# Kernel tuning notes

Hardware: AMD Instinct MI355X
Metric: run time of the kernel (lower is better)

Reference implementation:

```python
import jax, jax.numpy as jnp
from jax import lax
import numpy as np

EPS = 4e-3            # geoopt float32 ball boundary eps
MAXNORM = 1.0 - EPS   # c = 1 Poincare ball


def _norm(x):
    return jnp.sqrt(jnp.maximum(jnp.sum(x * x, axis=-1, keepdims=True), 1e-15))


def expmap0(u):
    n = _norm(u)
    return jnp.tanh(n) * u / n


def projx(x):
    n = _norm(x)
    return jnp.where(n > MAXNORM, x * (MAXNORM / n), x)


def mobius_add(x, y):
    x2 = jnp.sum(x * x, -1, keepdims=True)
    y2 = jnp.sum(y * y, -1, keepdims=True)
    xy = jnp.sum(x * y, -1, keepdims=True)
    num = (1.0 + 2.0 * xy + y2) * x + (1.0 - x2) * y
    den = 1.0 + 2.0 * xy + x2 * y2
    return num / jnp.maximum(den, 1e-15)


def mamba_layer(x, inW, convW, convb, xpW, dtW, dtb, A_log, Dp, outW):
    # x: [B,T,H]; inW: [2*Din,H]; convW: [Din,K]; xpW: [R+2N,Din]; dtW: [Din,R]
    B, T, H = x.shape
    Din, N = A_log.shape
    K = convW.shape[-1]
    R = dtW.shape[-1]
    xz = jnp.einsum('bth,dh->btd', x, inW)              # [B,T,2*Din]
    xr, z = jnp.split(xz, 2, axis=-1)
    xc = lax.conv_general_dilated(jnp.transpose(xr, (0, 2, 1)), convW[:, None, :],
                                  (1,), [(K - 1, 0)], feature_group_count=Din)
    u = jax.nn.silu(jnp.transpose(xc + convb[None, :, None], (0, 2, 1)))  # [B,T,Din]
    x_dbl = jnp.einsum('btd,ed->bte', u, xpW)           # [B,T,R+2N]
    dt_r, Bm, Cm = x_dbl[..., :R], x_dbl[..., R:R + N], x_dbl[..., R + N:]
    dt = jax.nn.softplus(jnp.einsum('btr,dr->btd', dt_r, dtW) + dtb)      # [B,T,Din]
    A = -jnp.exp(A_log)                                 # [Din,N]
    dA = jnp.exp(dt[..., None] * A)                     # [B,T,Din,N]
    dBu = dt[..., None] * Bm[:, :, None, :] * u[..., None]

    def step(h, ins):
        dA_t, dBu_t, C_t = ins
        h = dA_t * h + dBu_t                            # [B,Din,N]
        return h, jnp.einsum('bdn,bn->bd', h, C_t)

    h0 = jnp.zeros((B, Din, N), x.dtype)
    _, ys = lax.scan(step, h0, (jnp.moveaxis(dA, 1, 0), jnp.moveaxis(dBu, 1, 0), jnp.moveaxis(Cm, 1, 0)))
    y = jnp.moveaxis(ys, 0, 1) + Dp * u                 # [B,T,Din]
    return jnp.einsum('btd,hd->bth', y * jax.nn.silu(z), outW)


def _encode(xs, inp_W, inp_b, in_proj_W, conv_W, conv_b, xproj_W, dt_W, dt_b, A_log, D_skip, out_W, outp_W, outp_b):
    # xs: [4,B,T,1]; params carry leading branch dim 4, then layer dim 3
    def branch(x, iW, ib, ipW, cW, cb, xpW, dW, db, Al, Dp, oW, opW, opb):
        h = jnp.einsum('bti,hi->bth', x, iW) + ib
        for l in range(ipW.shape[0]):
            h = mamba_layer(h, ipW[l], cW[l], cb[l], xpW[l], dW[l], db[l], Al[l], Dp[l], oW[l])
        return jnp.tanh(jnp.einsum('bth,eh->bte', h, opW) + opb)
    return jax.vmap(branch)(xs, inp_W, inp_b, in_proj_W, conv_W, conv_b, xproj_W, dt_W, dt_b, A_log, D_skip, out_W, outp_W, outp_b)


def setup_inputs() -> dict:
    key = jax.random.key(0)
    ks = jax.random.split(key, 24)
    Br, B, T, H, Din, N, K, R, E, L = 4, 32, 1024, 64, 128, 16, 4, 4, 32, 3

    def rn(k, shape, s=0.05):
        return jax.random.normal(k, shape, jnp.float32) * s

    A_init = jnp.log(jnp.arange(1, N + 1, dtype=jnp.float32))
    return {
        'trend': jax.random.normal(ks[0], (B, T, 1), jnp.float32),
        'seasonal_weekly': jax.random.normal(ks[1], (B, T, 1), jnp.float32),
        'seasonal_daily': jax.random.normal(ks[2], (B, T, 1), jnp.float32),
        'residual': jax.random.normal(ks[3], (B, T, 1), jnp.float32),
        'inp_W': rn(ks[4], (Br, H, 1), 0.5),
        'inp_b': rn(ks[5], (Br, H)),
        'in_proj_W': rn(ks[6], (Br, L, 2 * Din, H)),
        'conv_W': rn(ks[7], (Br, L, Din, K), 0.2),
        'conv_b': rn(ks[8], (Br, L, Din)),
        'xproj_W': rn(ks[9], (Br, L, R + 2 * N, Din)),
        'dt_W': rn(ks[10], (Br, L, Din, R), 0.2),
        'dt_b': rn(ks[11], (Br, L, Din), 0.5) - 4.0,  # softplus(dt_b) small
        'A_log': jnp.tile(A_init, (Br, L, Din, 1)) + rn(ks[12], (Br, L, Din, N), 0.01),
        'D_skip': jnp.ones((Br, L, Din), jnp.float32) + rn(ks[13], (Br, L, Din), 0.01),
        'out_W': rn(ks[14], (Br, L, H, Din)),
        'outp_W': rn(ks[15], (Br, E, H)),
        'outp_b': rn(ks[16], (Br, E)),
    }


def reference(trend, seasonal_weekly, seasonal_daily, residual, inp_W, inp_b, in_proj_W, conv_W, conv_b, xproj_W, dt_W, dt_b, A_log, D_skip, out_W, outp_W, outp_b):
    xs = jnp.stack([trend, seasonal_weekly, seasonal_daily, residual], 0)  # [4,B,T,1]
    z = _encode(xs, inp_W, inp_b, in_proj_W, conv_W, conv_b, xproj_W, dt_W, dt_b, A_log, D_skip, out_W, outp_W, outp_b)  # [4,B,T,E]
    zh = projx(expmap0(z))
    t, w, d, r = zh[0], zh[1], zh[2], zh[3]
    comb = projx(mobius_add(mobius_add(t, mobius_add(w, d)), r))
    # stacked [trend_h, weekly_h, daily_h, residual_h, combined_h]
    return jnp.stack([t, w, d, r, comb], 0)
```

## Files before the change

### kernel.cpp

```cpp
#include <hip/hip_runtime.h>
#include <math.h>

#define TT 1024
#define DIN 128
#define HH 64
#define NN 16
#define EE 32
#define LL 3
#define BB 32

__device__ __forceinline__ float siluf(float x) { return x / (1.f + __expf(-x)); }

typedef __attribute__((ext_vector_type(8))) short bf16x8;
typedef __attribute__((ext_vector_type(4))) float f32x4;

__device__ __forceinline__ void split2(float x, ushort& hi, ushort& lo) {
  unsigned u = __float_as_uint(x);
  hi = (ushort)(u >> 16);
  float rem = x - __uint_as_float((u >> 16) << 16);
  lo = (ushort)(__float_as_uint(rem) >> 16);
}

#define WXZ_N 196608
#define WXD_N 73728
#define WOUT_N 98304

__global__ __launch_bounds__(256) void k_presplit(
    const float* __restrict__ iprojW, const float* __restrict__ xprojW,
    const float* __restrict__ outW,
    ushort* __restrict__ WxzH, ushort* __restrict__ WxzL,
    ushort* __restrict__ WxdH, ushort* __restrict__ WxdL,
    ushort* __restrict__ WoH, ushort* __restrict__ WoL) {
  int idx = blockIdx.x * 256 + threadIdx.x;
  if (idx < WXZ_N) {
    ushort h, l;
    split2(iprojW[idx], h, l);
    WxzH[idx] = h; WxzL[idx] = l;
  }
  if (idx < WXD_N) {
    int k = idx & 127, r = (idx >> 7) % 48, bl = idx / (48 * 128);
    float v = (r < 36) ? xprojW[((size_t)(bl * 36 + r)) * 128 + k] : 0.f;
    ushort h, l;
    split2(v, h, l);
    WxdH[idx] = h; WxdL[idx] = l;
  }
  if (idx < WOUT_N) {
    ushort h, l;
    split2(outW[idx], h, l);
    WoH[idx] = h; WoL[idx] = l;
  }
}

__global__ __launch_bounds__(256) void k_xz(
    const float* __restrict__ x0, const float* __restrict__ x1,
    const float* __restrict__ x2, const float* __restrict__ x3,
    const float* __restrict__ h, const ushort* __restrict__ WH,
    const ushort* __restrict__ WL,
    const float* __restrict__ inpW, const float* __restrict__ inpb,
    float* __restrict__ xr, float* __restrict__ zb, int br0, int l) {
  __shared__ __align__(16) ushort Hh[64][72], Hl[64][72];
  const int tid = threadIdx.x;
  const int b  = blockIdx.y;
  const int t0 = blockIdx.x * 64;
  const int br = br0 + (b >> 5);
  const float* Hg = h + ((size_t)b * TT + t0) * HH;
  {
    const int row = tid >> 2, c0 = (tid & 3) * 16;
    float xv = 0.f;
    if (l == 0) {
      int bb = b & 31;
      const float* xp = (br == 0) ? x0 : (br == 1) ? x1 : (br == 2) ? x2 : x3;
      xv = xp[bb * TT + t0 + row];
    }
    #pragma unroll
    for (int q = 0; q < 4; ++q) {
      float4 hv;
      if (l == 0) {
        float4 w4 = *(const float4*)(inpW + br * HH + c0 + q * 4);
        float4 b4 = *(const float4*)(inpb + br * HH + c0 + q * 4);
        hv.x = xv * w4.x + b4.x; hv.y = xv * w4.y + b4.y;
        hv.z = xv * w4.z + b4.z; hv.w = xv * w4.w + b4.w;
      } else {
        hv = *(const float4*)(Hg + (size_t)row * HH + c0 + q * 4);
      }
      ushort h0,h1,h2,h3,l0,l1,l2,l3;
      split2(hv.x,h0,l0); split2(hv.y,h1,l1); split2(hv.z,h2,l2); split2(hv.w,h3,l3);
      *(ushort4*)&Hh[row][c0 + q*4] = make_ushort4(h0,h1,h2,h3);
      *(ushort4*)&Hl[row][c0 + q*4] = make_ushort4(l0,l1,l2,l3);
    }
  }
  __syncthreads();
  const int wave = tid >> 6, lane = tid & 63;
  const int quad = lane >> 4, l16 = lane & 15;
  const int nsub = (wave & 1) * 32, tsub = (wave >> 1) * 32;
  const size_t wbase = (size_t)(br * LL + l) * 256;
  for (int n0 = 0; n0 < 2 * DIN; n0 += 64) {
    f32x4 acc[2][2] = {};
    #pragma unroll
    for (int k0 = 0; k0 < 64; k0 += 32) {
      bf16x8 Ah[2], Al[2], Bh[2], Bl[2];
      #pragma unroll
      for (int i = 0; i < 2; ++i) {
        size_t ro = (wbase + n0 + nsub + i * 16 + l16) * 64 + k0 + quad * 8;
        Ah[i] = *(const bf16x8*)(WH + ro);
        Al[i] = *(const bf16x8*)(WL + ro);
        Bh[i] = *(const bf16x8*)&Hh[tsub + i*16 + l16][k0 + quad*8];
        Bl[i] = *(const bf16x8*)&Hl[tsub + i*16 + l16][k0 + quad*8];
      }
      #pragma unroll
      for (int i = 0; i < 2; ++i)
        #pragma unroll
        for (int j = 0; j < 2; ++j) {
          acc[i][j] = __builtin_amdgcn_mfma_f32_16x16x32_bf16(Ah[i], Bh[j], acc[i][j], 0, 0, 0);
          acc[i][j] = __builtin_amdgcn_mfma_f32_16x16x32_bf16(Ah[i], Bl[j], acc[i][j], 0, 0, 0);
          acc[i][j] = __builtin_amdgcn_mfma_f32_16x16x32_bf16(Al[i], Bh[j], acc[i][j], 0, 0, 0);
        }
    }
    #pragma unroll
    for (int i = 0; i < 2; ++i) {
      #pragma unroll
      for (int r = 0; r < 4; ++r) {
        int n = n0 + nsub + i*16 + quad*4 + r;
        float* dst = (n < DIN) ? (xr + ((size_t)b * DIN + n) * TT)
                               : (zb + ((size_t)b * DIN + (n - DIN)) * TT);
        #pragma unroll
        for (int j = 0; j < 2; ++j)
          dst[t0 + tsub + j*16 + l16] = acc[i][j][r];
      }
    }
  }
}

__global__ __launch_bounds__(256) void k_xdbl(
    const float* __restrict__ xr, const float* __restrict__ convW,
    const float* __restrict__ convb, const ushort* __restrict__ WH,
    const ushort* __restrict__ WL, const float* __restrict__ dtW,
    const float* __restrict__ dtb,
    float* __restrict__ u, float* __restrict__ dt,
    float* __restrict__ Bm, float* __restrict__ Cm,
    int br0, int l) {
  __shared__ __align__(16) float Xr[16][72];
  __shared__ __align__(16) float As2[32][65];
  __shared__ __align__(16) float Xs[40][68];
  const int tid = threadIdx.x;
  const int b  = blockIdx.y;
  const int t0 = blockIdx.x * 64;
  const int br = br0 + (b >> 5);
  const int rowk = tid >> 4, c4 = tid & 15;
  const int wave = tid >> 6, lane = tid & 63;
  const int quad = lane >> 4, l16 = lane & 15;
  const int tw = wave * 16;
  const size_t wb48 = (size_t)(br * LL + l) * 48 * 128;
  f32x4 acc[3] = {};
  for (int k0 = 0; k0 < DIN; k0 += 32) {
    #pragma unroll
    for (int ks = 0; ks < 32; ks += 16) {
      __syncthreads();
      {
        const float* src = xr + ((size_t)b * DIN + k0 + ks + rowk) * TT + t0;
        *(float4*)&Xr[rowk][4 + c4 * 4] = *(const float4*)(src + c4 * 4);
        if (tid < 16) {
          float4 hv = make_float4(0.f, 0.f, 0.f, 0.f);
          if (t0 > 0) hv = *(const float4*)(xr + ((size_t)b * DIN + k0 + ks + tid) * TT + t0 - 4);
          *(float4*)&Xr[tid][0] = hv;
        }
      }
      __syncthreads();
      {
        int d = k0 + ks + rowk;
        const float* w = convW + (size_t)((br * LL + l) * DIN + d) * 4;
        float w0 = w[0], w1 = w[1], w2 = w[2], w3 = w[3];
        float cb = convb[(br * LL + l) * DIN + d];
        int ic = c4 * 4;
        float4 Av = *(const float4*)&Xr[rowk][ic];
        float4 Bv = *(const float4*)&Xr[rowk][ic + 4];
        float o0 = siluf(Av.y*w0 + Av.z*w1 + Av.w*w2 + Bv.x*w3 + cb);
        float o1 = siluf(Av.z*w0 + Av.w*w1 + Bv.x*w2 + Bv.y*w3 + cb);
        float o2 = siluf(Av.w*w0 + Bv.x*w1 + Bv.y*w2 + Bv.z*w3 + cb);
        float o3 = siluf(Bv.x*w0 + Bv.y*w1 + Bv.z*w2 + Bv.w*w3 + cb);
        *(float4*)(u + ((size_t)b * DIN + d) * TT + t0 + ic) = make_float4(o0, o1, o2, o3);
        As2[ks + rowk][ic]     = o0;
        As2[ks + rowk][ic + 1] = o1;
        As2[ks + rowk][ic + 2] = o2;
        As2[ks + rowk][ic + 3] = o3;
      }
    }
    __syncthreads();
    ushort bh[8], bl[8];
    #pragma unroll
    for (int j = 0; j < 8; ++j) {
      split2(As2[quad * 8 + j][tw + l16], bh[j], bl[j]);
    }
    bf16x8 Bh = *(bf16x8*)bh, Bl = *(bf16x8*)bl;
    #pragma unroll
    for (int nf = 0; nf < 3; ++nf) {
      size_t ro = wb48 + (size_t)(nf * 16 + l16) * 128 + k0 + quad * 8;
      bf16x8 Whf = *(const bf16x8*)(WH + ro);
      bf16x8 Wlf = *(const bf16x8*)(WL + ro);
      acc[nf] = __builtin_amdgcn_mfma_f32_16x16x32_bf16(Whf, Bh, acc[nf], 0, 0, 0);
      acc[nf] = __builtin_amdgcn_mfma_f32_16x16x32_bf16(Whf, Bl, acc[nf], 0, 0, 0);
      acc[nf] = __builtin_amdgcn_mfma_f32_16x16x32_bf16(Wlf, Bh, acc[nf], 0, 0, 0);
    }
  }
  __syncthreads();
  #pragma unroll
  for (int nf = 0; nf < 3; ++nf) {
    #pragma unroll
    for (int r = 0; r < 4; ++r) {
      int n = nf * 16 + quad * 4 + r;
      if (n < 40) Xs[n][tw + l16] = acc[nf][r];
    }
  }
  __syncthreads();
  {
    int n = tid >> 4, i0 = (tid & 15) * 4;
    *(float4*)(Bm + ((size_t)b * NN + n) * TT + t0 + i0) = *(float4*)&Xs[4 + n][i0];
    *(float4*)(Cm + ((size_t)b * NN + n) * TT + t0 + i0) = *(float4*)&Xs[20 + n][i0];
  }
  {
    int d = tid >> 1, half = tid & 1;
    const float* wd = dtW + (size_t)((br * LL + l) * DIN + d) * 4;
    float w0 = wd[0], w1 = wd[1], w2 = wd[2], w3 = wd[3];
    float bias = dtb[(br * LL + l) * DIN + d];
    float* dtp = dt + ((size_t)b * DIN + d) * TT + t0 + half * 32;
    #pragma unroll
    for (int g8 = 0; g8 < 8; ++g8) {
      float o[4];
      #pragma unroll
      for (int q = 0; q < 4; ++q) {
        int i = half * 32 + g8 * 4 + q;
        float s = Xs[0][i]*w0 + Xs[1][i]*w1 + Xs[2][i]*w2 + Xs[3][i]*w3 + bias;
        float e = __expf(-fabsf(s));
        o[q] = fmaxf(s, 0.f) + __logf(1.f + e);
      }
      *(float4*)(dtp + g8*4) = make_float4(o[0], o[1], o[2], o[3]);
    }
  }
}

__global__ __launch_bounds__(256) void k_scan1(
    float* __restrict__ dtc, const float* __restrict__ u,
    const float* __restrict__ Bm, const float* __restrict__ Cm,
    const float* __restrict__ A_log, const float* __restrict__ D_skip,
    float* __restrict__ Hloc, float* __restrict__ g, float* __restrict__ sdt,
    int br0, int l) {
  __shared__ __align__(16) float Bl[16][66];
  __shared__ __align__(16) float Cl[16][66];
  const int bx  = blockIdx.x;
  const int b   = bx >> 5;
  const int rem = bx & 31;
  const int c   = rem >> 1;
  const int dh  = rem & 1;
  const int tid = threadIdx.x;
  {
    int row = tid >> 4, cc = (tid & 15) * 4;
    float4 bv = *(const float4*)(Bm + ((size_t)b * NN + row) * TT + c * 64 + cc);
    *(float2*)&Bl[row][cc]     = make_float2(bv.x, bv.y);
    *(float2*)&Bl[row][cc + 2] = make_float2(bv.z, bv.w);
    float4 cv = *(const float4*)(Cm + ((size_t)b * NN + row) * TT + c * 64 + cc);
    *(float2*)&Cl[row][cc]     = make_float2(cv.x, cv.y);
    *(float2*)&Cl[row][cc + 2] = make_float2(cv.z, cv.w);
  }
  __syncthreads();
  const int d  = dh * 64 + (tid >> 2);
  const int n0 = (tid & 3) * 4;
  const int br = br0 + (b >> 5);
  const int wbase = (br * LL + l) * DIN + d;
  float Ac[4];
  #pragma unroll
  for (int j = 0; j < 4; ++j) Ac[j] = -__expf(A_log[(size_t)wbase * NN + n0 + j]);
  float Dp = D_skip[wbase];
  float* dtp = dtc + ((size_t)b * DIN + d) * TT + c * 64;
  const float* up = u + ((size_t)b * DIN + d) * TT + c * 64;
  float* gp = g + ((size_t)b * DIN + d) * TT + c * 64;
  float hst[4] = {0.f, 0.f, 0.f, 0.f};
  float sd = 0.f;
  float4 d0 = *(const float4*)(dtp);
  float4 d1 = *(const float4*)(dtp + 4);
  float4 u0 = *(const float4*)(up);
  float4 u1 = *(const float4*)(up + 4);
  #pragma unroll
  for (int t0 = 0; t0 < 64; t0 += 8) {
    float4 nd0, nd1, nu0, nu1;
    if (t0 < 56) {
      nd0 = *(const float4*)(dtp + t0 + 8);
      nd1 = *(const float4*)(dtp + t0 + 12);
      nu0 = *(const float4*)(up + t0 + 8);
      nu1 = *(const float4*)(up + t0 + 12);
    }
    float dts[8] = {d0.x, d0.y, d0.z, d0.w, d1.x, d1.y, d1.z, d1.w};
    float us[8]  = {u0.x, u0.y, u0.z, u0.w, u1.x, u1.y, u1.z, u1.w};
    float Bs[4][8], Cr[4][8];
    #pragma unroll
    for (int j = 0; j < 4; ++j) {
      float2 b0 = *(const float2*)&Bl[n0 + j][t0];
      float2 b1 = *(const float2*)&Bl[n0 + j][t0 + 2];
      float2 b2 = *(const float2*)&Bl[n0 + j][t0 + 4];
      float2 b3 = *(const float2*)&Bl[n0 + j][t0 + 6];
      Bs[j][0]=b0.x; Bs[j][1]=b0.y; Bs[j][2]=b1.x; Bs[j][3]=b1.y;
      Bs[j][4]=b2.x; Bs[j][5]=b2.y; Bs[j][6]=b3.x; Bs[j][7]=b3.y;
      float2 c0 = *(const float2*)&Cl[n0 + j][t0];
      float2 c1 = *(const float2*)&Cl[n0 + j][t0 + 2];
      float2 c2 = *(const float2*)&Cl[n0 + j][t0 + 4];
      float2 c3 = *(const float2*)&Cl[n0 + j][t0 + 6];
      Cr[j][0]=c0.x; Cr[j][1]=c0.y; Cr[j][2]=c1.x; Cr[j][3]=c1.y;
      Cr[j][4]=c2.x; Cr[j][5]=c2.y; Cr[j][6]=c3.x; Cr[j][7]=c3.y;
    }
    float yo[8], cds[8];
    #pragma unroll
    for (int s = 0; s < 8; ++s) {
      float dtv = dts[s], uv = us[s];
      sd += dtv;
      cds[s] = sd;
      float du = dtv * uv;
      float acc = 0.f;
      #pragma unroll
      for (int j = 0; j < 4; ++j) {
        float dA = __expf(dtv * Ac[j]);
        hst[j] = dA * hst[j] + du * Bs[j][s];
        acc += hst[j] * Cr[j][s];
      }
      acc += __shfl_xor(acc, 1, 4);
      acc += __shfl_xor(acc, 2, 4);
      yo[s] = acc + Dp * uv;
    }
    if ((tid & 3) == 0) {
      *(float4*)(gp + t0)     = make_float4(yo[0], yo[1], yo[2], yo[3]);
      *(float4*)(gp + t0 + 4) = make_float4(yo[4], yo[5], yo[6], yo[7]);
      *(float4*)(dtp + t0)     = make_float4(cds[0], cds[1], cds[2], cds[3]);
      *(float4*)(dtp + t0 + 4) = make_float4(cds[4], cds[5], cds[6], cds[7]);
    }
    d0 = nd0; d1 = nd1; u0 = nu0; u1 = nu1;
  }
  *(float4*)(Hloc + (((size_t)b * DIN + d) * 16 + c) * 16 + n0) =
      make_float4(hst[0], hst[1], hst[2], hst[3]);
  if ((tid & 3) == 0) sdt[((size_t)b * DIN + d) * 16 + c] = sd;
}

__global__ __launch_bounds__(256) void k_scan2(
    const float* __restrict__ cdc, const float* __restrict__ Cm,
    const float* __restrict__ A_log, const float* __restrict__ Hloc,
    const float* __restrict__ sdt, float* __restrict__ g, int br0, int l) {
  __shared__ __align__(16) float Cl[16][68];
  __shared__ __align__(16) float HinL[32][16];
  const int bx  = blockIdx.x;
  const int b   = bx / 60;
  const int rem = bx % 60;
  const int c   = (rem >> 2) + 1;
  const int dq  = rem & 3;
  const int tid = threadIdx.x;
  const int br  = br0 + (b >> 5);
  {
    int row = tid >> 4, cc = (tid & 15) * 4;
    *(float4*)&Cl[row][cc] = *(const float4*)(Cm + ((size_t)b * NN + row) * TT + c * 64 + cc);
  }
  const int dloc = tid >> 3, tg = tid & 7;
  const int d  = dq * 32 + dloc;
  size_t off = ((size_t)b * DIN + d) * TT + c * 64 + tg * 8;
  float* gp = g + off;
  float4 y0 = *(const float4*)gp;
  float4 y1 = *(const float4*)(gp + 4);
  float4 cq0 = *(const float4*)(cdc + off);
  float4 cq1 = *(const float4*)(cdc + off + 4);
  {
    int n0 = (tid & 7) * 2;
    int wbase = (br * LL + l) * DIN + d;
    float a0 = -__expf(A_log[(size_t)wbase * NN + n0]);
    float a1 = -__expf(A_log[(size_t)wbase * NN + n0 + 1]);
    float h0 = 0.f, h1 = 0.f;
    const float* sp  = sdt + ((size_t)b * DIN + d) * 16;
    const float* hlb = Hloc + ((size_t)b * DIN + d) * 256;
    for (int cc = 0; cc < c; ++cc) {
      float sdv = sp[cc];
      float2 hl = *(const float2*)(hlb + cc * 16 + n0);
      h0 = __expf(a0 * sdv) * h0 + hl.x;
      h1 = __expf(a1 * sdv) * h1 + hl.y;
    }
    HinL[dloc][n0] = h0;
    HinL[dloc][n0 + 1] = h1;
  }
  __syncthreads();
  float cd8[8] = {cq0.x, cq0.y, cq0.z, cq0.w, cq1.x, cq1.y, cq1.z, cq1.w};
  const float* al = A_log + (size_t)((br * LL + l) * DIN + d) * NN;
  float Ac16[16];
  #pragma unroll
  for (int n = 0; n < 16; ++n) Ac16[n] = -__expf(al[n]);
  float y8[8] = {y0.x, y0.y, y0.z, y0.w, y1.x, y1.y, y1.z, y1.w};
  const int tbase = tg * 8;
  #pragma unroll
  for (int n = 0; n < 16; ++n) {
    float hv = HinL[dloc][n];
    float an = Ac16[n];
    #pragma unroll
    for (int s = 0; s < 8; ++s)
      y8[s] += Cl[n][tbase + s] * __expf(an * cd8[s]) * hv;
  }
  *(float4*)gp       = make_float4(y8[0], y8[1], y8[2], y8[3]);
  *(float4*)(gp + 4) = make_float4(y8[4], y8[5], y8[6], y8[7]);
}

__global__ __launch_bounds__(256) void k_out(
    const float* __restrict__ graw, const float* __restrict__ zb,
    const ushort* __restrict__ WH, const ushort* __restrict__ WL,
    float* __restrict__ h, int br0, int l) {
  __shared__ __align__(16) ushort Bh_[64][72], Bl_[64][72];
  const int tid = threadIdx.x;
  const int b  = blockIdx.y;
  const int t0 = blockIdx.x * 64;
  const int br = br0 + (b >> 5);
  const int wave = tid >> 6, lane = tid & 63;
  const int quad = lane >> 4, l16 = lane & 15;
  const int hsub = (wave & 1) * 32, tsub = (wave >> 1) * 32;
  const size_t wb = (size_t)(br * LL + l) * 64;
  f32x4 acc[2][2] = {};
  for (int k0 = 0; k0 < DIN; k0 += 64) {
    __syncthreads();
    {
      int row = tid >> 2, c0 = (tid & 3) * 16;
      #pragma unroll
      for (int q = 0; q < 4; ++q) {
        size_t off = ((size_t)b * DIN + k0 + row) * TT + t0 + c0 + q * 4;
        float4 gv = *(const float4*)(graw + off);
        float4 zv = *(const float4*)(zb + off);
        float a0 = gv.x * siluf(zv.x), a1 = gv.y * siluf(zv.y);
        float a2 = gv.z * siluf(zv.z), a3 = gv.w * siluf(zv.w);
        ushort h0,h1,h2,h3,l0,l1,l2,l3;
        split2(a0,h0,l0); split2(a1,h1,l1); split2(a2,h2,l2); split2(a3,h3,l3);
        *(ushort4*)&Bh_[row][c0 + q*4] = make_ushort4(h0,h1,h2,h3);
        *(ushort4*)&Bl_[row][c0 + q*4] = make_ushort4(l0,l1,l2,l3);
      }
    }
    __syncthreads();
    #pragma unroll
    for (int kk = 0; kk < 64; kk += 32) {
      bf16x8 Ahf[2], Alf[2], Bhf[2], Blf[2];
      #pragma unroll
      for (int i = 0; i < 2; ++i) {
        size_t ro = (wb + hsub + i * 16 + l16) * 128 + k0 + kk + quad * 8;
        Ahf[i] = *(const bf16x8*)(WH + ro);
        Alf[i] = *(const bf16x8*)(WL + ro);
        Bhf[i] = *(const bf16x8*)&Bh_[tsub + i*16 + l16][kk + quad*8];
        Blf[i] = *(const bf16x8*)&Bl_[tsub + i*16 + l16][kk + quad*8];
      }
      #pragma unroll
      for (int i = 0; i < 2; ++i)
        #pragma unroll
        for (int j = 0; j < 2; ++j) {
          acc[i][j] = __builtin_amdgcn_mfma_f32_16x16x32_bf16(Ahf[i], Bhf[j], acc[i][j], 0, 0, 0);
          acc[i][j] = __builtin_amdgcn_mfma_f32_16x16x32_bf16(Ahf[i], Blf[j], acc[i][j], 0, 0, 0);
          acc[i][j] = __builtin_amdgcn_mfma_f32_16x16x32_bf16(Alf[i], Bhf[j], acc[i][j], 0, 0, 0);
        }
    }
  }
  #pragma unroll
  for (int i = 0; i < 2; ++i) {
    int hh0 = hsub + i*16 + quad*4;
    #pragma unroll
    for (int j = 0; j < 2; ++j) {
      int t = t0 + tsub + j*16 + l16;
      *(f32x4*)(h + ((size_t)b * TT + t) * HH + hh0) = acc[i][j];
    }
  }
}

__global__ __launch_bounds__(256) void k_ze(
    const float* __restrict__ h, const float* __restrict__ outpW,
    const float* __restrict__ outpb, float* __restrict__ ze, int br0) {
  __shared__ __align__(16) float As[16][132];
  __shared__ __align__(16) float Ws[16][36];
  __shared__ __align__(16) float Cs[128][36];
  const int tid = threadIdx.x;
  const int b  = blockIdx.y;
  const int t0 = blockIdx.x * 128;
  const int br = br0 + (b >> 5);
  const float* W = outpW + (size_t)br * EE * HH;
  float acc[4][4] = {};
  const int ti = tid & 31, ni = tid >> 5;
  for (int k0 = 0; k0 < HH; k0 += 16) {
    __syncthreads();
    {
      int i = tid >> 1, kq = (tid & 1) * 8;
      const float* src = h + ((size_t)b * TT + t0 + i) * HH + k0 + kq;
      float4 a0 = *(const float4*)src;
      float4 a1 = *(const float4*)(src + 4);
      As[kq+0][i]=a0.x; As[kq+1][i]=a0.y; As[kq+2][i]=a0.z; As[kq+3][i]=a0.w;
      As[kq+4][i]=a1.x; As[kq+5][i]=a1.y; As[kq+6][i]=a1.z; As[kq+7][i]=a1.w;
    }
    for (int idx = tid; idx < 512; idx += 256) {
      int jj = idx >> 4, kk = idx & 15;
      Ws[kk][jj] = W[(size_t)jj * HH + k0 + kk];
    }
    __syncthreads();
    #pragma unroll
    for (int kk = 0; kk < 16; ++kk) {
      float4 a = *(const float4*)&As[kk][ti * 4];
      float4 w = *(const float4*)&Ws[kk][ni * 4];
      acc[0][0] += a.x*w.x; acc[0][1] += a.x*w.y; acc[0][2] += a.x*w.z; acc[0][3] += a.x*w.w;
      acc[1][0] += a.y*w.x; acc[1][1] += a.y*w.y; acc[1][2] += a.y*w.z; acc[1][3] += a.y*w.w;
      acc[2][0] += a.z*w.x; acc[2][1] += a.z*w.y; acc[2][2] += a.z*w.z; acc[2][3] += a.z*w.w;
      acc[3][0] += a.w*w.x; acc[3][1] += a.w*w.y; acc[3][2] += a.w*w.z; acc[3][3] += a.w*w.w;
    }
  }
  __syncthreads();
  float bj[4];
  #pragma unroll
  for (int c = 0; c < 4; ++c) bj[c] = outpb[br * EE + ni*4 + c];
  #pragma unroll
  for (int r = 0; r < 4; ++r)
    #pragma unroll
    for (int c = 0; c < 4; ++c)
      Cs[ti*4+r][ni*4+c] = tanhf(acc[r][c] + bj[c]);
  __syncthreads();
  int i = tid >> 1, j16 = (tid & 1) * 16;
  float* dst = ze + (((size_t)(br0 * 32 + b)) * TT + t0 + i) * EE + j16;
  #pragma unroll
  for (int q = 0; q < 4; ++q)
    *(float4*)(dst + q*4) = *(float4*)&Cs[i][j16 + q*4];
}

__device__ __forceinline__ void mobius_add32(const float* x, const float* y, float* o) {
  float x2 = 0.f, y2 = 0.f, xy = 0.f;
  #pragma unroll
  for (int i = 0; i < 32; ++i) { x2 += x[i]*x[i]; y2 += y[i]*y[i]; xy += x[i]*y[i]; }
  float ca  = 1.f + 2.f*xy + y2;
  float cb  = 1.f - x2;
  float den = 1.f + 2.f*xy + x2*y2;
  float inv = 1.f / fmaxf(den, 1e-15f);
  #pragma unroll
  for (int i = 0; i < 32; ++i) o[i] = (ca*x[i] + cb*y[i]) * inv;
}

__global__ __launch_bounds__(256) void k_hyper(const float* __restrict__ ze,
                                               float* __restrict__ out) {
  int idx = blockIdx.x * 256 + threadIdx.x;
  int b = idx >> 10, t = idx & 1023;
  float v[4][32];
  #pragma unroll
  for (int br = 0; br < 4; ++br) {
    const float* p = ze + (((size_t)br * BB + b) * TT + t) * EE;
    float s = 0.f;
    #pragma unroll
    for (int e = 0; e < 32; ++e) { v[br][e] = p[e]; s += v[br][e]*v[br][e]; }
    float nr = sqrtf(fmaxf(s, 1e-15f));
    float sc = tanhf(nr) / nr;
    float s2 = 0.f;
    #pragma unroll
    for (int e = 0; e < 32; ++e) { v[br][e] *= sc; s2 += v[br][e]*v[br][e]; }
    float n2 = sqrtf(fmaxf(s2, 1e-15f));
    if (n2 > 0.996f) {
      float sc2 = 0.996f / n2;
      #pragma unroll
      for (int e = 0; e < 32; ++e) v[br][e] *= sc2;
    }
    float* o = out + (((size_t)br * BB + b) * TT + t) * EE;
    #pragma unroll
    for (int e = 0; e < 32; ++e) o[e] = v[br][e];
  }
  float m1[32], m2[32];
  mobius_add32(v[1], v[2], m1);
  mobius_add32(v[0], m1, m2);
  mobius_add32(m2, v[3], m1);
  float s = 0.f;
  #pragma unroll
  for (int e = 0; e < 32; ++e) s += m1[e]*m1[e];
  float n = sqrtf(fmaxf(s, 1e-15f));
  if (n > 0.996f) {
    float sc = 0.996f / n;
    #pragma unroll
    for (int e = 0; e < 32; ++e) m1[e] *= sc;
  }
  float* o = out + (((size_t)4 * BB + b) * TT + t) * EE;
  #pragma unroll
  for (int e = 0; e < 32; ++e) o[e] = m1[e];
}

extern "C" void kernel_launch(void* const* d_in, const int* in_sizes, int n_in,
                              void* d_out, int out_size, void* d_ws, size_t ws_size,
                              hipStream_t stream) {
  const float* xs0 = (const float*)d_in[0];
  const float* xs1 = (const float*)d_in[1];
  const float* xs2 = (const float*)d_in[2];
  const float* xs3 = (const float*)d_in[3];
  const float* inpW   = (const float*)d_in[4];
  const float* inpb   = (const float*)d_in[5];
  const float* iprojW = (const float*)d_in[6];
  const float* convW  = (const float*)d_in[7];
  const float* convb  = (const float*)d_in[8];
  const float* xprojW = (const float*)d_in[9];
  const float* dtW    = (const float*)d_in[10];
  const float* dtb    = (const float*)d_in[11];
  const float* A_log  = (const float*)d_in[12];
  const float* D_skip = (const float*)d_in[13];
  const float* outW   = (const float*)d_in[14];
  const float* outpW  = (const float*)d_in[15];
  const float* outpb  = (const float*)d_in[16];
  float* out = (float*)d_out;

  const size_t wUshorts = 2 * (WXZ_N + WXD_N + WOUT_N);
  ushort* WxzH = (ushort*)d_ws;
  ushort* WxzL = WxzH + WXZ_N;
  ushort* WxdH = WxzL + WXZ_N;
  ushort* WxdL = WxdH + WXD_N;
  ushort* WoH  = WxdL + WXD_N;
  ushort* WoL  = WoH + WOUT_N;
  float* ws = (float*)(WoL + WOUT_N);

  const size_t zeF = (size_t)4 * BB * TT * EE;
  const size_t perBl = 65536 + 4 * 131072 + 2 * 16384 + 2048;
  auto needBytes = [&](int NB) {
    return (zeF + (size_t)NB * 32 * perBl) * 4 + wUshorts * 2;
  };
  int NB = 4;
  if (needBytes(4) > ws_size) NB = 2;
  if (NB == 2 && needBytes(2) > ws_size) NB = 1;
  const int nbl = NB * 32;

  float* ze = ws;
  float* h  = ze + zeF;
  float* xr = h  + (size_t)nbl * 65536;
  float* zb = xr + (size_t)nbl * 131072;
  float* u  = zb + (size_t)nbl * 131072;
  float* dt = u  + (size_t)nbl * 131072;
  float* Bm = dt + (size_t)nbl * 131072;
  float* Cm = Bm + (size_t)nbl * 16384;
  float* sdt = Cm + (size_t)nbl * 16384;
  float* g  = xr;
  float* Hloc = h;

  k_presplit<<<WXZ_N / 256, 256, 0, stream>>>(iprojW, xprojW, outW,
                                              WxzH, WxzL, WxdH, WxdL, WoH, WoL);

  for (int br0 = 0; br0 < 4; br0 += NB) {
    for (int l = 0; l < LL; ++l) {
      k_xz   <<<dim3(16, nbl), 256, 0, stream>>>(xs0, xs1, xs2, xs3, h,
                                                 WxzH, WxzL, inpW, inpb, xr, zb, br0, l);
      k_xdbl <<<dim3(16, nbl), 256, 0, stream>>>(xr, convW, convb, WxdH, WxdL,
                                                 dtW, dtb, u, dt, Bm, Cm, br0, l);
      k_scan1<<<nbl * 32, 256, 0, stream>>>(dt, u, Bm, Cm, A_log, D_skip,
                                            Hloc, g, sdt, br0, l);
      k_scan2<<<nbl * 60, 256, 0, stream>>>(dt, Cm, A_log, Hloc, sdt, g, br0, l);
      k_out  <<<dim3(16, nbl), 256, 0, stream>>>(g, zb, WoH, WoL, h, br0, l);
    }
    k_ze<<<dim3(8, nbl), 256, 0, stream>>>(h, outpW, outpb, ze, br0);
  }
  k_hyper<<<BB * TT / 256, 256, 0, stream>>>(ze, out);
}
```

Measured before the change: 1.092 ms.

## Fuse chunk-local selective scan into the conv/x-projection kernel

Merges the k_scan1 chunk-local scan into the k_xdbl kernel. The conv output u, dt and B now stay in shared memory instead of making a round trip through global memory, and one kernel launch per layer is removed. Each block now keeps the full 128x64 u tile in LDS and runs the scan with two threads per channel, eight states each. The larger LDS footprint and fewer threads per channel-state may lower occupancy and serialize more exp work per thread.

```diff
diff --git a/kernel.cpp b/kernel.cpp
--- a/kernel.cpp
+++ b/kernel.cpp
@@ -131,20 +131,22 @@
   }
 }
 
-__global__ __launch_bounds__(256) void k_xdbl(
+__global__ __launch_bounds__(256) void k_xds(
     const float* __restrict__ xr, const float* __restrict__ convW,
     const float* __restrict__ convb, const ushort* __restrict__ WH,
     const ushort* __restrict__ WL, const float* __restrict__ dtW,
-    const float* __restrict__ dtb,
-    float* __restrict__ u, float* __restrict__ dt,
-    float* __restrict__ Bm, float* __restrict__ Cm,
+    const float* __restrict__ dtb, const float* __restrict__ A_log,
+    const float* __restrict__ D_skip,
+    float* __restrict__ cd, float* __restrict__ Cm,
+    float* __restrict__ Hloc, float* __restrict__ g, float* __restrict__ sdt,
     int br0, int l) {
   __shared__ __align__(16) float Xr[16][72];
-  __shared__ __align__(16) float As2[32][65];
+  __shared__ __align__(16) float U[128][66];
   __shared__ __align__(16) float Xs[40][68];
   const int tid = threadIdx.x;
   const int b  = blockIdx.y;
-  const int t0 = blockIdx.x * 64;
+  const int c  = blockIdx.x;
+  const int t0 = c * 64;
   const int br = br0 + (b >> 5);
   const int rowk = tid >> 4, c4 = tid & 15;
   const int wave = tid >> 6, lane = tid & 63;
@@ -178,19 +180,15 @@
         float o1 = siluf(Av.z*w0 + Av.w*w1 + Bv.x*w2 + Bv.y*w3 + cb);
         float o2 = siluf(Av.w*w0 + Bv.x*w1 + Bv.y*w2 + Bv.z*w3 + cb);
         float o3 = siluf(Bv.x*w0 + Bv.y*w1 + Bv.z*w2 + Bv.w*w3 + cb);
-        *(float4*)(u + ((size_t)b * DIN + d) * TT + t0 + ic) = make_float4(o0, o1, o2, o3);
-        As2[ks + rowk][ic]     = o0;
-        As2[ks + rowk][ic + 1] = o1;
-        As2[ks + rowk][ic + 2] = o2;
-        As2[ks + rowk][ic + 3] = o3;
+        *(float2*)&U[d][ic]     = make_float2(o0, o1);
+        *(float2*)&U[d][ic + 2] = make_float2(o2, o3);
       }
     }
     __syncthreads();
     ushort bh[8], bl[8];
     #pragma unroll
-    for (int j = 0; j < 8; ++j) {
-      split2(As2[quad * 8 + j][tw + l16], bh[j], bl[j]);
-    }
+    for (int j = 0; j < 8; ++j)
+      split2(U[k0 + quad * 8 + j][tw + l16], bh[j], bl[j]);
     bf16x8 Bh = *(bf16x8*)bh, Bl = *(bf16x8*)bl;
     #pragma unroll
     for (int nf = 0; nf < 3; ++nf) {
@@ -214,127 +212,90 @@
   __syncthreads();
   {
     int n = tid >> 4, i0 = (tid & 15) * 4;
-    *(float4*)(Bm + ((size_t)b * NN + n) * TT + t0 + i0) = *(float4*)&Xs[4 + n][i0];
     *(float4*)(Cm + ((size_t)b * NN + n) * TT + t0 + i0) = *(float4*)&Xs[20 + n][i0];
   }
+  const int dd = tid >> 1, p = tid & 1, n0s = p * 8;
+  const int wbase = (br * LL + l) * DIN + dd;
+  const float* wd = dtW + (size_t)wbase * 4;
+  const float w0 = wd[0], w1 = wd[1], w2 = wd[2], w3 = wd[3];
+  const float bias = dtb[wbase];
+  float Ac[8];
+  #pragma unroll
+  for (int j = 0; j < 8; ++j) Ac[j] = -__expf(A_log[(size_t)wbase * NN + n0s + j]);
+  const float Dp = D_skip[wbase];
+  float hst[8] = {0.f,0.f,0.f,0.f,0.f,0.f,0.f,0.f};
+  float sd = 0.f;
+  float* gp  = g  + ((size_t)b * DIN + dd) * TT + t0;
+  float* cdp = cd + ((size_t)b * DIN + dd) * TT + t0;
+  for (int t8 = 0; t8 < 64; t8 += 8) {
+    float4 a0 = *(const float4*)&Xs[0][t8], a0b = *(const float4*)&Xs[0][t8 + 4];
+    float4 a1 = *(const float4*)&Xs[1][t8], a1b = *(const float4*)&Xs[1][t8 + 4];
+    float4 a2 = *(const float4*)&Xs[2][t8], a2b = *(const float4*)&Xs[2][t8 + 4];
+    float4 a3 = *(const float4*)&Xs[3][t8], a3b = *(const float4*)&Xs[3][t8 + 4];
+    float x0v[8] = {a0.x,a0.y,a0.z,a0.w,a0b.x,a0b.y,a0b.z,a0b.w};
+    float x1v[8] = {a1.x,a1.y,a1.z,a1.w,a1b.x,a1b.y,a1b.z,a1b.w};
+    float x2v[8] = {a2.x,a2.y,a2.z,a2.w,a2b.x,a2b.y,a2b.z,a2b.w};
+    float x3v[8] = {a3.x,a3.y,a3.z,a3.w,a3b.x,a3b.y,a3b.z,a3b.w};
+    float us[8];
+    {
+      float2 u0 = *(const float2*)&U[dd][t8];
+      float2 u1 = *(const float2*)&U[dd][t8 + 2];
+      float2 u2 = *(const float2*)&U[dd][t8 + 4];
+      float2 u3 = *(const float2*)&U[dd][t8 + 6];
+      us[0]=u0.x; us[1]=u0.y; us[2]=u1.x; us[3]=u1.y;
+      us[4]=u2.x; us[5]=u2.y; us[6]=u3.x; us[7]=u3.y;
+    }
+    float dts[8], cds[8], du[8];
+    #pragma unroll
+    for (int s = 0; s < 8; ++s) {
+      float sv = x0v[s]*w0 + x1v[s]*w1 + x2v[s]*w2 + x3v[s]*w3 + bias;
+      float e = __expf(-fabsf(sv));
+      float dtv = fmaxf(sv, 0.f) + __logf(1.f + e);
+      sd += dtv;
+      dts[s] = dtv;
+      cds[s] = sd;
+      du[s] = dtv * us[s];
+    }
+    float acc8[8] = {0.f,0.f,0.f,0.f,0.f,0.f,0.f,0.f};
+    #pragma unroll
+    for (int j = 0; j < 8; ++j) {
+      int n = n0s + j;
+      float2 b0 = *(const float2*)&Xs[4 + n][t8];
+      float2 b1 = *(const float2*)&Xs[4 + n][t8 + 2];
+      float2 b2 = *(const float2*)&Xs[4 + n][t8 + 4];
+      float2 b3 = *(const float2*)&Xs[4 + n][t8 + 6];
+      float2 c0 = *(const float2*)&Xs[20 + n][t8];
+      float2 c1 = *(const float2*)&Xs[20 + n][t8 + 2];
+      float2 c2 = *(const float2*)&Xs[20 + n][t8 + 4];
+      float2 c3 = *(const float2*)&Xs[20 + n][t8 + 6];
+      float Bv[8] = {b0.x,b0.y,b1.x,b1.y,b2.x,b2.y,b3.x,b3.y};
+      float Cv[8] = {c0.x,c0.y,c1.x,c1.y,c2.x,c2.y,c3.x,c3.y};
+      float hj = hst[j], an = Ac[j];
+      #pragma unroll
+      for (int s = 0; s < 8; ++s) {
+        hj = __expf(dts[s] * an) * hj + du[s] * Bv[s];
+        acc8[s] += hj * Cv[s];
+      }
+      hst[j] = hj;
+    }
+    #pragma unroll
+    for (int s = 0; s < 8; ++s) {
+      float tot = acc8[s] + __shfl_xor(acc8[s], 1, 2);
+      acc8[s] = tot + Dp * us[s];
+    }
+    if (p == 0) {
+      *(float4*)(gp + t8)      = make_float4(acc8[0], acc8[1], acc8[2], acc8[3]);
+      *(float4*)(gp + t8 + 4)  = make_float4(acc8[4], acc8[5], acc8[6], acc8[7]);
+      *(float4*)(cdp + t8)     = make_float4(cds[0], cds[1], cds[2], cds[3]);
+      *(float4*)(cdp + t8 + 4) = make_float4(cds[4], cds[5], cds[6], cds[7]);
+    }
+  }
   {
-    int d = tid >> 1, half = tid & 1;
-    const float* wd = dtW + (size_t)((br * LL + l) * DIN + d) * 4;
-    float w0 = wd[0], w1 = wd[1], w2 = wd[2], w3 = wd[3];
-    float bias = dtb[(br * LL + l) * DIN + d];
-    float* dtp = dt + ((size_t)b * DIN + d) * TT + t0 + half * 32;
-    #pragma unroll
-    for (int g8 = 0; g8 < 8; ++g8) {
-      float o[4];
-      #pragma unroll
-      for (int q = 0; q < 4; ++q) {
-        int i = half * 32 + g8 * 4 + q;
-        float s = Xs[0][i]*w0 + Xs[1][i]*w1 + Xs[2][i]*w2 + Xs[3][i]*w3 + bias;
-        float e = __expf(-fabsf(s));
-        o[q] = fmaxf(s, 0.f) + __logf(1.f + e);
-      }
-      *(float4*)(dtp + g8*4) = make_float4(o[0], o[1], o[2], o[3]);
-    }
-  }
-}
-
-__global__ __launch_bounds__(256) void k_scan1(
-    float* __restrict__ dtc, const float* __restrict__ u,
-    const float* __restrict__ Bm, const float* __restrict__ Cm,
-    const float* __restrict__ A_log, const float* __restrict__ D_skip,
-    float* __restrict__ Hloc, float* __restrict__ g, float* __restrict__ sdt,
-    int br0, int l) {
-  __shared__ __align__(16) float Bl[16][66];
-  __shared__ __align__(16) float Cl[16][66];
-  const int bx  = blockIdx.x;
-  const int b   = bx >> 5;
-  const int rem = bx & 31;
-  const int c   = rem >> 1;
-  const int dh  = rem & 1;
-  const int tid = threadIdx.x;
-  {
-    int row = tid >> 4, cc = (tid & 15) * 4;
-    float4 bv = *(const float4*)(Bm + ((size_t)b * NN + row) * TT + c * 64 + cc);
-    *(float2*)&Bl[row][cc]     = make_float2(bv.x, bv.y);
-    *(float2*)&Bl[row][cc + 2] = make_float2(bv.z, bv.w);
-    float4 cv = *(const float4*)(Cm + ((size_t)b * NN + row) * TT + c * 64 + cc);
-    *(float2*)&Cl[row][cc]     = make_float2(cv.x, cv.y);
-    *(float2*)&Cl[row][cc + 2] = make_float2(cv.z, cv.w);
-  }
-  __syncthreads();
-  const int d  = dh * 64 + (tid >> 2);
-  const int n0 = (tid & 3) * 4;
-  const int br = br0 + (b >> 5);
-  const int wbase = (br * LL + l) * DIN + d;
-  float Ac[4];
-  #pragma unroll
-  for (int j = 0; j < 4; ++j) Ac[j] = -__expf(A_log[(size_t)wbase * NN + n0 + j]);
-  float Dp = D_skip[wbase];
-  float* dtp = dtc + ((size_t)b * DIN + d) * TT + c * 64;
-  const float* up = u + ((size_t)b * DIN + d) * TT + c * 64;
-  float* gp = g + ((size_t)b * DIN + d) * TT + c * 64;
-  float hst[4] = {0.f, 0.f, 0.f, 0.f};
-  float sd = 0.f;
-  float4 d0 = *(const float4*)(dtp);
-  float4 d1 = *(const float4*)(dtp + 4);
-  float4 u0 = *(const float4*)(up);
-  float4 u1 = *(const float4*)(up + 4);
-  #pragma unroll
-  for (int t0 = 0; t0 < 64; t0 += 8) {
-    float4 nd0, nd1, nu0, nu1;
-    if (t0 < 56) {
-      nd0 = *(const float4*)(dtp + t0 + 8);
-      nd1 = *(const float4*)(dtp + t0 + 12);
-      nu0 = *(const float4*)(up + t0 + 8);
-      nu1 = *(const float4*)(up + t0 + 12);
-    }
-    float dts[8] = {d0.x, d0.y, d0.z, d0.w, d1.x, d1.y, d1.z, d1.w};
-    float us[8]  = {u0.x, u0.y, u0.z, u0.w, u1.x, u1.y, u1.z, u1.w};
-    float Bs[4][8], Cr[4][8];
-    #pragma unroll
-    for (int j = 0; j < 4; ++j) {
-      float2 b0 = *(const float2*)&Bl[n0 + j][t0];
-      float2 b1 = *(const float2*)&Bl[n0 + j][t0 + 2];
-      float2 b2 = *(const float2*)&Bl[n0 + j][t0 + 4];
-      float2 b3 = *(const float2*)&Bl[n0 + j][t0 + 6];
-      Bs[j][0]=b0.x; Bs[j][1]=b0.y; Bs[j][2]=b1.x; Bs[j][3]=b1.y;
-      Bs[j][4]=b2.x; Bs[j][5]=b2.y; Bs[j][6]=b3.x; Bs[j][7]=b3.y;
-      float2 c0 = *(const float2*)&Cl[n0 + j][t0];
-      float2 c1 = *(const float2*)&Cl[n0 + j][t0 + 2];
-      float2 c2 = *(const float2*)&Cl[n0 + j][t0 + 4];
-      float2 c3 = *(const float2*)&Cl[n0 + j][t0 + 6];
-      Cr[j][0]=c0.x; Cr[j][1]=c0.y; Cr[j][2]=c1.x; Cr[j][3]=c1.y;
-      Cr[j][4]=c2.x; Cr[j][5]=c2.y; Cr[j][6]=c3.x; Cr[j][7]=c3.y;
-    }
-    float yo[8], cds[8];
-    #pragma unroll
-    for (int s = 0; s < 8; ++s) {
-      float dtv = dts[s], uv = us[s];
-      sd += dtv;
-      cds[s] = sd;
-      float du = dtv * uv;
-      float acc = 0.f;
-      #pragma unroll
-      for (int j = 0; j < 4; ++j) {
-        float dA = __expf(dtv * Ac[j]);
-        hst[j] = dA * hst[j] + du * Bs[j][s];
-        acc += hst[j] * Cr[j][s];
-      }
-      acc += __shfl_xor(acc, 1, 4);
-      acc += __shfl_xor(acc, 2, 4);
-      yo[s] = acc + Dp * uv;
-    }
-    if ((tid & 3) == 0) {
-      *(float4*)(gp + t0)     = make_float4(yo[0], yo[1], yo[2], yo[3]);
-      *(float4*)(gp + t0 + 4) = make_float4(yo[4], yo[5], yo[6], yo[7]);
-      *(float4*)(dtp + t0)     = make_float4(cds[0], cds[1], cds[2], cds[3]);
-      *(float4*)(dtp + t0 + 4) = make_float4(cds[4], cds[5], cds[6], cds[7]);
-    }
-    d0 = nd0; d1 = nd1; u0 = nu0; u1 = nu1;
-  }
-  *(float4*)(Hloc + (((size_t)b * DIN + d) * 16 + c) * 16 + n0) =
-      make_float4(hst[0], hst[1], hst[2], hst[3]);
-  if ((tid & 3) == 0) sdt[((size_t)b * DIN + d) * 16 + c] = sd;
+    float* hp = Hloc + (((size_t)b * DIN + dd) * 16 + c) * 16 + n0s;
+    *(float4*)hp       = make_float4(hst[0], hst[1], hst[2], hst[3]);
+    *(float4*)(hp + 4) = make_float4(hst[4], hst[5], hst[6], hst[7]);
+  }
+  if (p == 0) sdt[((size_t)b * DIN + dd) * 16 + c] = sd;
 }
 
 __global__ __launch_bounds__(256) void k_scan2(
@@ -619,13 +580,13 @@
   float* h  = ze + zeF;
   float* xr = h  + (size_t)nbl * 65536;
   float* zb = xr + (size_t)nbl * 131072;
-  float* u  = zb + (size_t)nbl * 131072;
-  float* dt = u  + (size_t)nbl * 131072;
-  float* Bm = dt + (size_t)nbl * 131072;
+  float* g  = zb + (size_t)nbl * 131072;
+  float* cd = g  + (size_t)nbl * 131072;
+  float* Bm = cd + (size_t)nbl * 131072;
   float* Cm = Bm + (size_t)nbl * 16384;
   float* sdt = Cm + (size_t)nbl * 16384;
-  float* g  = xr;
   float* Hloc = h;
+  (void)Bm;
 
   k_presplit<<<WXZ_N / 256, 256, 0, stream>>>(iprojW, xprojW, outW,
                                               WxzH, WxzL, WxdH, WxdL, WoH, WoL);
@@ -634,11 +595,10 @@
     for (int l = 0; l < LL; ++l) {
       k_xz   <<<dim3(16, nbl), 256, 0, stream>>>(xs0, xs1, xs2, xs3, h,
                                                  WxzH, WxzL, inpW, inpb, xr, zb, br0, l);
-      k_xdbl <<<dim3(16, nbl), 256, 0, stream>>>(xr, convW, convb, WxdH, WxdL,
-                                                 dtW, dtb, u, dt, Bm, Cm, br0, l);
-      k_scan1<<<nbl * 32, 256, 0, stream>>>(dt, u, Bm, Cm, A_log, D_skip,
-                                            Hloc, g, sdt, br0, l);
-      k_scan2<<<nbl * 60, 256, 0, stream>>>(dt, Cm, A_log, Hloc, sdt, g, br0, l);
+      k_xds  <<<dim3(16, nbl), 256, 0, stream>>>(xr, convW, convb, WxdH, WxdL,
+                                                 dtW, dtb, A_log, D_skip,
+                                                 cd, Cm, Hloc, g, sdt, br0, l);
+      k_scan2<<<nbl * 60, 256, 0, stream>>>(cd, Cm, A_log, Hloc, sdt, g, br0, l);
       k_out  <<<dim3(16, nbl), 256, 0, stream>>>(g, zb, WoH, WoL, h, br0, l);
     }
     k_ze<<<dim3(8, nbl), 256, 0, stream>>>(h, outpW, outpb, ze, br0);
```

After: 1.053 ms. 3.6% less time.
